# Optimization experiments

Measured on AMD Instinct MI355X. Metric: run time of the kernel, lower is better.

The kernel has to match this reference:

```python
import jax, jax.numpy as jnp
import numpy as np

EMBED = 768
DIM = 800          # embed + 32 gender features
IN_C = 1024
GRID = 32          # img_size // patch_size(=1)
LN_EPS = 1e-5      # torch nn.LayerNorm default


def setup_inputs() -> dict:
    key = jax.random.key(0)
    ks = jax.random.split(key, 8)
    B = 32
    x = jax.random.normal(ks[0], (B, IN_C, GRID, GRID), dtype=jnp.float32)
    gender_encode = jax.random.normal(ks[1], (B, 32), dtype=jnp.float32)
    # PatchEmbed 1x1 conv (acts as per-pixel linear) + LayerNorm params
    conv_w = jax.random.normal(ks[2], (EMBED, IN_C), dtype=jnp.float32) * (IN_C ** -0.5)
    conv_b = jnp.zeros((EMBED,), dtype=jnp.float32)
    ln_g = jnp.ones((EMBED,), dtype=jnp.float32)
    ln_b = jnp.zeros((EMBED,), dtype=jnp.float32)
    cls_token = jax.random.normal(ks[3], (1, 1, EMBED), dtype=jnp.float32) * 0.02
    # Attention qkv linear (bias=True); proj is never used in the forward path
    qkv_w = jax.random.normal(ks[4], (3 * DIM, DIM), dtype=jnp.float32) * (DIM ** -0.5)
    qkv_b = jnp.zeros((3 * DIM,), dtype=jnp.float32)
    return {
        "x": x, "gender_encode": gender_encode,
        "conv_w": conv_w, "conv_b": conv_b,
        "ln_g": ln_g, "ln_b": ln_b,
        "cls_token": cls_token,
        "qkv_w": qkv_w, "qkv_b": qkv_b,
    }


def _forward(x, gender_encode, conv_w, conv_b, ln_g, ln_b, cls_token, qkv_w, qkv_b):
    B = x.shape[0]
    # PatchEmbed: 1x1 conv stride 1 == per-pixel linear; flatten(2).transpose(1,2)
    p = jnp.einsum('bchw,oc->bhwo', x, conv_w) + conv_b        # [B,32,32,768]
    p = p.reshape(B, GRID * GRID, EMBED)                        # [B,1024,768]
    mu = jnp.mean(p, axis=-1, keepdims=True)
    var = jnp.mean((p - mu) ** 2, axis=-1, keepdims=True)
    p = (p - mu) * jax.lax.rsqrt(var + LN_EPS) * ln_g + ln_b
    # prepend cls token, concat broadcast gender features
    cls = jnp.broadcast_to(cls_token, (B, 1, EMBED))
    t = jnp.concatenate([cls, p], axis=1)                       # [B,1025,768]
    g = jnp.broadcast_to(gender_encode[:, None, :], (B, t.shape[1], 32))
    t = jnp.concatenate([t, g], axis=2)                         # [B,1025,800]
    # Attention (note: self.norm / proj / v are unused in the original forward)
    qkv = t @ qkv_w.T + qkv_b                                   # [B,1025,2400]
    q = qkv[..., 0:DIM]
    k = qkv[..., DIM:2 * DIM]
    scale = DIM ** -0.5
    # only the cls-query row is ever used -> compute just that row
    scores = jnp.einsum('bc,bnc->bn', q[:, 0], k) * scale       # [B,1025]
    attn_cls = jax.nn.softmax(scores[:, 1:], axis=-1)           # [B,1024]
    return attn_cls.reshape(B, 1, GRID, GRID)


def reference(x, gender_encode, conv_w, conv_b, ln_g, ln_b, cls_token, qkv_w, qkv_b):
    return _forward(x, gender_encode, conv_w, conv_b, ln_g, ln_b, cls_token, qkv_w, qkv_b)
```

## Files before the change

### kernel.cpp

```cpp
#include <hip/hip_runtime.h>
#include <hip/hip_bf16.h>

#define EMBED 768
#define DIMQ  800
#define INC   1024
#define NPIX  1024

typedef __bf16 bf16_t;
typedef __bf16 bf16x8 __attribute__((ext_vector_type(8)));
typedef float  f32x4  __attribute__((ext_vector_type(4)));

#define GLD_LDS(gp, lp) __builtin_amdgcn_global_load_lds( \
    (const __attribute__((address_space(1))) void*)(gp),  \
    (__attribute__((address_space(3))) void*)(lp), 16, 0, 0)

__global__ __launch_bounds__(256)
void k_prep(const float* __restrict__ x, bf16_t* __restrict__ xT,
            const float* __restrict__ w, bf16_t* __restrict__ cw,
            const float* __restrict__ qkv_w, const float* __restrict__ qkv_b,
            const float* __restrict__ cls, const float* __restrict__ gender,
            float* __restrict__ q0b) {
    __shared__ __align__(16) float tile[64 * 64];
    const int bi = blockIdx.x;
    const int t  = threadIdx.x;
    if (bi < 8192) {
        const int b  = bi >> 8;
        const int k0 = ((bi >> 4) & 15) * 64;
        const int m0 = (bi & 15) * 64;
        {
            const int kl = t >> 4;
            const int mq = t & 15;
#pragma unroll
            for (int r = 0; r < 4; ++r) {
                const int k = r * 16 + kl;
                f32x4 v = *(const f32x4*)(x + ((size_t)(b * 1024 + k0 + k) * 1024) + m0 + mq * 4);
                const int f = ((k >> 3) + (k & 7)) & 15;
                *(f32x4*)&tile[k * 64 + ((mq ^ f) & 15) * 4] = v;
            }
        }
        __syncthreads();
        {
            const int j    = t & 7;
            const int mrow = t >> 3;
#pragma unroll
            for (int rep = 0; rep < 2; ++rep) {
                const int m = mrow + rep * 32;
                bf16x8 pk;
#pragma unroll
                for (int i = 0; i < 8; ++i) {
                    const int k = j * 8 + i;
                    const int f = ((k >> 3) + (k & 7)) & 15;
                    pk[i] = (bf16_t)tile[k * 64 + (((m >> 2) ^ f) & 15) * 4 + (m & 3)];
                }
                const int slot = j ^ (m & 7);
                *(bf16x8*)(xT + ((size_t)(b * 1024 + m0 + m) * 1024) + k0 + slot * 8) = pk;
            }
        }
    } else if (bi < 8392) {
        const int wv = t >> 6, tl = t & 63;
        const int i = (bi - 8192) * 4 + wv;
        const float* row = qkv_w + (size_t)i * DIMQ;
        float ps = 0.f;
        for (int j = tl; j < EMBED; j += 64) ps += row[j] * cls[j];
#pragma unroll
        for (int off = 1; off < 64; off <<= 1) ps += __shfl_xor(ps, off, 64);
        if (tl < 32) {
            float g = 0.f;
#pragma unroll
            for (int j = 0; j < 32; ++j) g += row[EMBED + j] * gender[tl * 32 + j];
            q0b[tl * DIMQ + i] = ps + g + qkv_b[i];
        }
    } else {
        const int i = (bi - 8392) * 256 + t;
        const int n = i >> 10, k = i & 1023;
        const int s = (k >> 3) & 7;
        const int src_k = (k & ~63) | (((s ^ (n & 7)) & 7) << 3) | (k & 7);
        cw[i] = (bf16_t)w[(size_t)n * 1024 + src_k];
    }
}

__global__ __launch_bounds__(1024)
void k_u(const float* __restrict__ qkv_w, const float* __restrict__ q0b,
         const float* __restrict__ ln_g, float* __restrict__ u) {
    __shared__ float wk_s[160 * 32];
    __shared__ float q0_s[160 * 33];
    const int t  = threadIdx.x;
    const int j0 = blockIdx.x * 32;
    const int jj = t >> 5, b = t & 31;
    const float* wk = qkv_w + (size_t)DIMQ * DIMQ;
    float acc0 = 0.f, acc1 = 0.f;
    for (int c = 0; c < 5; ++c) {
        const int o0 = c * 160;
        __syncthreads();
#pragma unroll
        for (int i = 0; i < 5; ++i) {
            const int idx = i * 1024 + t;
            const int o  = idx >> 5, jl = idx & 31;
            wk_s[o * 32 + jl] = wk[(size_t)(o0 + o) * DIMQ + j0 + jl];
            const int b2 = idx / 160, o2 = idx % 160;
            q0_s[o2 * 33 + b2] = q0b[b2 * DIMQ + o0 + o2];
        }
        __syncthreads();
#pragma unroll 8
        for (int o = 0; o < 160; o += 2) {
            acc0 += wk_s[o * 32 + jj]       * q0_s[o * 33 + b];
            acc1 += wk_s[(o + 1) * 32 + jj] * q0_s[(o + 1) * 33 + b];
        }
    }
    u[b * EMBED + j0 + jj] = (acc0 + acc1) * ln_g[j0 + jj];
}

__global__ __launch_bounds__(256, 3)
void k_main(const bf16_t* __restrict__ xT, const bf16_t* __restrict__ cw,
            const float* __restrict__ conv_b, const float* __restrict__ u,
            float* __restrict__ partial) {
    __shared__ __align__(1024) unsigned char smem[32768 + 3072];

    const int tid = threadIdx.x;
    const int bi = blockIdx.x;
    const int x8 = bi & 7;
    const int s  = bi >> 3;
    const int nt = s % 6;
    const int mt = (s / 6) * 8 + x8;
    const int b  = mt >> 3;
    const int gm = mt * 128;
    const int gn = nt * 128;

    const int wv = tid >> 6;
    const int l  = tid & 63;
    const int lr = l >> 3;
    const int lc = l & 7;

    const int lane = l;
    const int col  = lane & 15;
    const int quad = lane >> 4;
    const int wm   = (wv >> 1) * 64;
    const int wn   = (wv & 1) * 64;

    bf16_t* A = (bf16_t*)smem;
    bf16_t* B = (bf16_t*)(smem + 16384);

    f32x4 C[4][4] = {};

    for (int kt = 0; kt < 16; ++kt) {
        const int ko = kt * 64;
#pragma unroll
        for (int p = 0; p < 4; ++p) {
            const int r = p * 32 + wv * 8 + lr;
            GLD_LDS(xT + (size_t)(gm + r) * 1024 + ko + lc * 8, A + (p * 32 + wv * 8) * 64);
            GLD_LDS(cw + (size_t)(gn + r) * 1024 + ko + lc * 8, B + (p * 32 + wv * 8) * 64);
        }
        __syncthreads();
#pragma unroll
        for (int ks = 0; ks < 2; ++ks) {
            bf16x8 af[4], bg[4];
#pragma unroll
            for (int mi = 0; mi < 4; ++mi) {
                const int r  = wm + mi * 16 + col;
                const int ph = (ks * 4 + quad) ^ (r & 7);
                af[mi] = *(const bf16x8*)(A + r * 64 + ph * 8);
            }
#pragma unroll
            for (int ni = 0; ni < 4; ++ni) {
                const int r  = wn + ni * 16 + col;
                const int ph = (ks * 4 + quad) ^ (r & 7);
                bg[ni] = *(const bf16x8*)(B + r * 64 + ph * 8);
            }
#pragma unroll
            for (int mi = 0; mi < 4; ++mi)
#pragma unroll
                for (int ni = 0; ni < 4; ++ni)
                    C[mi][ni] = __builtin_amdgcn_mfma_f32_16x16x32_bf16(af[mi], bg[ni], C[mi][ni], 0, 0, 0);
        }
        __syncthreads();
    }

    float cb[4], uv[4];
#pragma unroll
    for (int ni = 0; ni < 4; ++ni) {
        const int og = gn + wn + ni * 16 + col;
        cb[ni] = conv_b[og];
        uv[ni] = u[b * EMBED + og];
    }
    float* part = (float*)(smem + 32768);
#pragma unroll
    for (int mi = 0; mi < 4; ++mi)
#pragma unroll
        for (int r = 0; r < 4; ++r) {
            float a = 0.f, sq = 0.f, d = 0.f;
#pragma unroll
            for (int ni = 0; ni < 4; ++ni) {
                float v = C[mi][ni][r] + cb[ni];
                a += v; sq += v * v; d += v * uv[ni];
            }
#pragma unroll
            for (int off = 1; off < 16; off <<= 1) {
                a  += __shfl_xor(a, off, 64);
                sq += __shfl_xor(sq, off, 64);
                d  += __shfl_xor(d, off, 64);
            }
            if (col == 0) {
                const int row = wm + mi * 16 + quad * 4 + r;
                float* pp = part + ((wv & 1) * 128 + row) * 3;
                pp[0] = a; pp[1] = sq; pp[2] = d;
            }
        }
    __syncthreads();
    if (tid < 128) {
        const float* p0 = part + tid * 3;
        const float* p1 = part + (128 + tid) * 3;
        const size_t pix = (size_t)gm + tid;
        partial[(size_t)(0 * 6 + nt) * 32768 + pix] = p0[0] + p1[0];
        partial[(size_t)(1 * 6 + nt) * 32768 + pix] = p0[1] + p1[1];
        partial[(size_t)(2 * 6 + nt) * 32768 + pix] = p0[2] + p1[2];
    }
}

__global__ __launch_bounds__(1024)
void k_final(const float* __restrict__ partial, const float* __restrict__ u,
             float* __restrict__ out) {
    __shared__ float red[16];
    __shared__ float bc[3];
    const int b = blockIdx.x, t = threadIdx.x;
    const int lane = t & 63, wid = t >> 6;

    float pu = (t < EMBED) ? u[b * EMBED + t] : 0.f;
#pragma unroll
    for (int off = 1; off < 64; off <<= 1) pu += __shfl_xor(pu, off, 64);
    if (lane == 0) red[wid] = pu;
    __syncthreads();
    if (t == 0) { float s = 0.f; for (int i = 0; i < 16; ++i) s += red[i]; bc[0] = s; }
    __syncthreads();
    const float Su = bc[0];

    const size_t m = (size_t)b * 1024 + t;
    float S1 = 0.f, S2 = 0.f, S3 = 0.f;
#pragma unroll
    for (int nt = 0; nt < 6; ++nt) {
        S1 += partial[(size_t)(0 * 6 + nt) * 32768 + m];
        S2 += partial[(size_t)(1 * 6 + nt) * 32768 + m];
        S3 += partial[(size_t)(2 * 6 + nt) * 32768 + m];
    }
    const float mu  = S1 * (1.f / 768.f);
    const float var = S2 * (1.f / 768.f) - mu * mu;
    const float sc  = 0.035355339059327376f * (S3 - mu * Su) * rsqrtf(var + 1e-5f);

    float mx = sc;
#pragma unroll
    for (int off = 1; off < 64; off <<= 1) mx = fmaxf(mx, __shfl_xor(mx, off, 64));
    if (lane == 0) red[wid] = mx;
    __syncthreads();
    if (t == 0) { float mm = -1e30f; for (int i = 0; i < 16; ++i) mm = fmaxf(mm, red[i]); bc[1] = mm; }
    __syncthreads();
    const float e = __expf(sc - bc[1]);
    float ss = e;
#pragma unroll
    for (int off = 1; off < 64; off <<= 1) ss += __shfl_xor(ss, off, 64);
    __syncthreads();
    if (lane == 0) red[wid] = ss;
    __syncthreads();
    if (t == 0) { float s = 0.f; for (int i = 0; i < 16; ++i) s += red[i]; bc[2] = s; }
    __syncthreads();
    out[m] = e / bc[2];
}

extern "C" void kernel_launch(void* const* d_in, const int* in_sizes, int n_in,
                              void* d_out, int out_size, void* d_ws, size_t ws_size,
                              hipStream_t stream) {
    const float* x      = (const float*)d_in[0];
    const float* gender = (const float*)d_in[1];
    const float* conv_w = (const float*)d_in[2];
    const float* conv_b = (const float*)d_in[3];
    const float* ln_g   = (const float*)d_in[4];
    const float* cls    = (const float*)d_in[6];
    const float* qkv_w  = (const float*)d_in[7];
    const float* qkv_b  = (const float*)d_in[8];
    float* out = (float*)d_out;

    char* ws = (char*)d_ws;
    bf16_t* cw      = (bf16_t*)ws;
    float*  q0b     = (float*)(ws + 1572864);
    float*  u       = (float*)(ws + 1675264);
    float*  partial = (float*)(ws + 1773568);
    bf16_t* xT      = (bf16_t*)(ws + 4132864);

    hipLaunchKernelGGL(k_prep,  dim3(11464), dim3(256),  0, stream,
                       x, xT, conv_w, cw, qkv_w, qkv_b, cls, gender, q0b);
    hipLaunchKernelGGL(k_u,     dim3(24),    dim3(1024), 0, stream, qkv_w, q0b, ln_g, u);
    hipLaunchKernelGGL(k_main,  dim3(1536),  dim3(256),  0, stream, xT, cw, conv_b, u, partial);
    hipLaunchKernelGGL(k_final, dim3(32),    dim3(1024), 0, stream, partial, u, out);
}
```

Measured before the change: 315.0 us.

## Double-buffer A tile in LDS and load B fragments directly into registers

The main GEMM now keeps the conv-weight (B) operand out of shared memory. Each wave loads its B fragments straight from global memory into registers, so the weight no longer needs the XOR swizzle in the prep kernel. The A (activation) tile is double-buffered across two LDS halves so the next k-step's global-to-LDS load overlaps the current MFMA work. This raises register pressure, so launch bounds drop to 2 blocks per CU, trading occupancy for overlap, and it adds redundant global reads of B across waves.

```diff
diff --git a/kernel.cpp b/kernel.cpp
--- a/kernel.cpp
+++ b/kernel.cpp
@@ -72,10 +72,7 @@
         }
     } else {
         const int i = (bi - 8392) * 256 + t;
-        const int n = i >> 10, k = i & 1023;
-        const int s = (k >> 3) & 7;
-        const int src_k = (k & ~63) | (((s ^ (n & 7)) & 7) << 3) | (k & 7);
-        cw[i] = (bf16_t)w[(size_t)n * 1024 + src_k];
+        cw[i] = (bf16_t)w[i];
     }
 }
 
@@ -110,7 +107,7 @@
     u[b * EMBED + j0 + jj] = (acc0 + acc1) * ln_g[j0 + jj];
 }
 
-__global__ __launch_bounds__(256, 3)
+__global__ __launch_bounds__(256, 2)
 void k_main(const bf16_t* __restrict__ xT, const bf16_t* __restrict__ cw,
             const float* __restrict__ conv_b, const float* __restrict__ u,
             float* __restrict__ partial) {
@@ -130,47 +127,88 @@
     const int l  = tid & 63;
     const int lr = l >> 3;
     const int lc = l & 7;
-
-    const int lane = l;
-    const int col  = lane & 15;
-    const int quad = lane >> 4;
+    const int col  = l & 15;
+    const int quad = l >> 4;
     const int wm   = (wv >> 1) * 64;
     const int wn   = (wv & 1) * 64;
 
-    bf16_t* A = (bf16_t*)smem;
-    bf16_t* B = (bf16_t*)(smem + 16384);
+    bf16_t* A0 = (bf16_t*)smem;
+    bf16_t* A1 = (bf16_t*)(smem + 16384);
+
+    const bf16_t* bp[4];
+#pragma unroll
+    for (int ni = 0; ni < 4; ++ni)
+        bp[ni] = cw + (size_t)(gn + wn + ni * 16 + col) * 1024 + quad * 8;
+
+    const bf16_t* ap = xT + (size_t)(gm + wv * 8 + lr) * 1024 + lc * 8;
+    const int aldso = (wv * 8) * 64;
 
     f32x4 C[4][4] = {};
-
-    for (int kt = 0; kt < 16; ++kt) {
-        const int ko = kt * 64;
-#pragma unroll
-        for (int p = 0; p < 4; ++p) {
-            const int r = p * 32 + wv * 8 + lr;
-            GLD_LDS(xT + (size_t)(gm + r) * 1024 + ko + lc * 8, A + (p * 32 + wv * 8) * 64);
-            GLD_LDS(cw + (size_t)(gn + r) * 1024 + ko + lc * 8, B + (p * 32 + wv * 8) * 64);
-        }
-        __syncthreads();
+    bf16x8 b0[2][4], b1[2][4];
+
+#pragma unroll
+    for (int ks = 0; ks < 2; ++ks)
+#pragma unroll
+        for (int ni = 0; ni < 4; ++ni)
+            b0[ks][ni] = *(const bf16x8*)(bp[ni] + ks * 32);
+#pragma unroll
+    for (int p = 0; p < 4; ++p)
+        GLD_LDS(ap + (size_t)(p * 32) * 1024, A0 + aldso + p * 2048);
+    __syncthreads();
+
+    for (int kt2 = 0; kt2 < 16; kt2 += 2) {
+        {
+            const int ko = (kt2 + 1) * 64;
+#pragma unroll
+            for (int p = 0; p < 4; ++p)
+                GLD_LDS(ap + (size_t)(p * 32) * 1024 + ko, A1 + aldso + p * 2048);
+#pragma unroll
+            for (int ks = 0; ks < 2; ++ks)
+#pragma unroll
+                for (int ni = 0; ni < 4; ++ni)
+                    b1[ks][ni] = *(const bf16x8*)(bp[ni] + ko + ks * 32);
+        }
 #pragma unroll
         for (int ks = 0; ks < 2; ++ks) {
-            bf16x8 af[4], bg[4];
+            bf16x8 af[4];
 #pragma unroll
             for (int mi = 0; mi < 4; ++mi) {
                 const int r  = wm + mi * 16 + col;
                 const int ph = (ks * 4 + quad) ^ (r & 7);
-                af[mi] = *(const bf16x8*)(A + r * 64 + ph * 8);
-            }
-#pragma unroll
-            for (int ni = 0; ni < 4; ++ni) {
-                const int r  = wn + ni * 16 + col;
+                af[mi] = *(const bf16x8*)(A0 + r * 64 + ph * 8);
+            }
+#pragma unroll
+            for (int mi = 0; mi < 4; ++mi)
+#pragma unroll
+                for (int ni = 0; ni < 4; ++ni)
+                    C[mi][ni] = __builtin_amdgcn_mfma_f32_16x16x32_bf16(af[mi], b0[ks][ni], C[mi][ni], 0, 0, 0);
+        }
+        __syncthreads();
+        if (kt2 + 2 < 16) {
+            const int ko = (kt2 + 2) * 64;
+#pragma unroll
+            for (int p = 0; p < 4; ++p)
+                GLD_LDS(ap + (size_t)(p * 32) * 1024 + ko, A0 + aldso + p * 2048);
+#pragma unroll
+            for (int ks = 0; ks < 2; ++ks)
+#pragma unroll
+                for (int ni = 0; ni < 4; ++ni)
+                    b0[ks][ni] = *(const bf16x8*)(bp[ni] + ko + ks * 32);
+        }
+#pragma unroll
+        for (int ks = 0; ks < 2; ++ks) {
+            bf16x8 af[4];
+#pragma unroll
+            for (int mi = 0; mi < 4; ++mi) {
+                const int r  = wm + mi * 16 + col;
                 const int ph = (ks * 4 + quad) ^ (r & 7);
-                bg[ni] = *(const bf16x8*)(B + r * 64 + ph * 8);
+                af[mi] = *(const bf16x8*)(A1 + r * 64 + ph * 8);
             }
 #pragma unroll
             for (int mi = 0; mi < 4; ++mi)
 #pragma unroll
                 for (int ni = 0; ni < 4; ++ni)
-                    C[mi][ni] = __builtin_amdgcn_mfma_f32_16x16x32_bf16(af[mi], bg[ni], C[mi][ni], 0, 0, 0);
+                    C[mi][ni] = __builtin_amdgcn_mfma_f32_16x16x32_bf16(af[mi], b1[ks][ni], C[mi][ni], 0, 0, 0);
         }
         __syncthreads();
     }
```

Measured after the change: 370.3 us. 17.6% more time.
